# Performance work log

Hardware: AMD Instinct MI355X
Metric: run time of the kernel (lower is better)

The kernel has to match this reference:

```python
import jax, jax.numpy as jnp
import numpy as np

B, H, S, D = 2, 16, 2048, 64
SOFTCLAMP = 50.0


def setup_inputs() -> dict:
    key = jax.random.key(0)
    kq, kk, kv, km = jax.random.split(key, 4)
    q = jax.random.normal(kq, (B, H, S, D), dtype=jnp.float32)
    k = jax.random.normal(kk, (B, H, S, D), dtype=jnp.float32)
    v = jax.random.normal(kv, (B, H, S, D), dtype=jnp.float32)
    mask = jax.random.randint(km, (B, S), 0, 2).astype(jnp.bool_)
    return {"q": q, "k": k, "v": v, "mask": mask}


def reference(q, k, v, mask):
    scale = q.shape[-1] ** -0.5
    # [b, h, i, j] similarity logits
    sim = jnp.einsum('bhid,bhjd->bhij', q, k) * scale
    # tanh-based logit softclamping (Gemma2-style softcapping)
    sim = jnp.tanh(sim / SOFTCLAMP) * SOFTCLAMP
    mask_value = -jnp.finfo(sim.dtype).max
    sim = jnp.where(mask[:, None, None, :], sim, mask_value)
    attn = jax.nn.softmax(sim, axis=-1)
    out = jnp.einsum('bhij,bhjd->bhid', attn, v)
    return out, attn
```

## Files before the change

### kernel.cpp

```cpp
#include <hip/hip_runtime.h>
#include <hip/hip_bf16.h>

#define B_ 2
#define H_ 16
#define S_ 2048
#define D_ 64
#define PSTR 2056

typedef float f32x4 __attribute__((ext_vector_type(4)));
typedef short s16x8 __attribute__((ext_vector_type(8)));
typedef short s16x4 __attribute__((ext_vector_type(4)));

__device__ __forceinline__ short f2bf(float f) {
  unsigned u = __float_as_uint(f);
  u += 0x7FFFu + ((u >> 16) & 1u);
  return (short)(u >> 16);
}
__device__ __forceinline__ float bf2f(short s) {
  return __uint_as_float(((unsigned)(unsigned short)s) << 16);
}

__device__ __forceinline__ float softcap_p(float a) {
  const float k1 = 0.18033688011f;
  const float k2 = -3.7570183e-07f;
  const float k3 = 9.3926761e-13f;
  const float C  = 72.134752044f;
  float y = a * a;
  float t = __builtin_fmaf(y, k3, k2);
  t = __builtin_fmaf(y, t, k1);
  float arg = __builtin_fmaf(a, t, -C);
  arg = fminf(arg, 0.f);
  return exp2f(arg);
}

__global__ __launch_bounds__(256) void prep_qk(const float* __restrict__ q,
                                               const float* __restrict__ k,
                                               short* __restrict__ qbf,
                                               short* __restrict__ kbf) {
  size_t i = ((size_t)blockIdx.x * 256 + threadIdx.x) * 8;
  const f32x4* qa = (const f32x4*)(q + i);
  const f32x4* ka = (const f32x4*)(k + i);
  f32x4 a0 = __builtin_nontemporal_load(qa);
  f32x4 a1 = __builtin_nontemporal_load(qa + 1);
  f32x4 b0 = __builtin_nontemporal_load(ka);
  f32x4 b1 = __builtin_nontemporal_load(ka + 1);
  s16x8 oq, ok;
  #pragma unroll
  for (int e = 0; e < 4; ++e) {
    oq[e] = f2bf(a0[e]); oq[4 + e] = f2bf(a1[e]);
    ok[e] = f2bf(b0[e]); ok[4 + e] = f2bf(b1[e]);
  }
  *(s16x8*)(qbf + i) = oq;
  *(s16x8*)(kbf + i) = ok;
}

__global__ __launch_bounds__(256) void prep_v(const float* __restrict__ v,
                                              short* __restrict__ vt) {
  __shared__ float tile[64][65];
  const int tid = threadIdx.x;
  const int j0 = blockIdx.x * 64;
  const int bh = blockIdx.y;
  const float* vh = v + (size_t)bh * S_ * D_;
  #pragma unroll
  for (int it = 0; it < 16; ++it) {
    int idx = it * 256 + tid;
    int row = idx >> 6, col = idx & 63;
    tile[row][col] = __builtin_nontemporal_load(&vh[(size_t)(j0 + row) * D_ + col]);
  }
  __syncthreads();
  short* vth = vt + (size_t)bh * D_ * S_;
  #pragma unroll
  for (int it = 0; it < 16; ++it) {
    int idx = it * 256 + tid;
    int d = idx >> 6, jj = idx & 63;
    vth[(size_t)d * S_ + j0 + jj] = f2bf(tile[jj][d]);
  }
}

template <bool PRE>
__global__ __launch_bounds__(512, 2) void attend_fused(
    const float* __restrict__ q, const float* __restrict__ k,
    const float* __restrict__ v, const int* __restrict__ mask,
    const short* __restrict__ qbf, const short* __restrict__ kbf,
    const short* __restrict__ vt,
    float* __restrict__ out, float* __restrict__ attn) {
  __shared__ short strip[16 * PSTR];
  __shared__ float ls_rs[8][16];
  __shared__ float ls_rinv[16];

  const int tid  = threadIdx.x;
  const int wv   = tid >> 6;
  const int lane = tid & 63;
  const int lg   = lane >> 4;
  const int li   = lane & 15;

  const unsigned flat = blockIdx.y * gridDim.x + blockIdx.x;
  const unsigned swz  = (flat & 7) * 512 + (flat >> 3);
  const int q0 = (int)(swz & 127) * 16;
  const int bh = (int)(swz >> 7);
  const int b  = bh >> 4;
  const int* mrow = mask + (size_t)b * S_;

  s16x8 qf0, qf1;
  if constexpr (PRE) {
    const short* qr = qbf + ((size_t)bh * S_ + q0 + li) * D_ + lg * 8;
    qf0 = *(const s16x8*)qr;
    qf1 = *(const s16x8*)(qr + 32);
  } else {
    const float* qr = q + ((size_t)bh * S_ + q0 + li) * D_ + lg * 8;
    #pragma unroll
    for (int e = 0; e < 8; ++e) { qf0[e] = f2bf(qr[e]); qf1[e] = f2bf(qr[32 + e]); }
  }

  const short* kbase = PRE ? (kbf + (size_t)bh * S_ * D_) : nullptr;
  s16x8 kf[8];
  auto ldK = [&](int cc) {
    const int jcc = cc * 512 + wv * 64;
    #pragma unroll
    for (int n = 0; n < 4; ++n) {
      const short* kr = kbase + (size_t)(jcc + n * 16 + li) * D_ + lg * 8;
      kf[2 * n]     = *(const s16x8*)kr;
      kf[2 * n + 1] = *(const s16x8*)(kr + 32);
    }
  };
  if constexpr (PRE) ldK(0);

  float rs[4] = {0.f, 0.f, 0.f, 0.f};
  f32x4 pvacc[4];
  #pragma unroll
  for (int m = 0; m < 4; ++m) pvacc[m] = (f32x4){0.f, 0.f, 0.f, 0.f};

  #pragma unroll
  for (int c = 0; c < 4; ++c) {
    const int jc = c * 512 + wv * 64;

    f32x4 acc[4];
    #pragma unroll
    for (int n = 0; n < 4; ++n) acc[n] = (f32x4){0.f, 0.f, 0.f, 0.f};
    if constexpr (PRE) {
      #pragma unroll
      for (int n = 0; n < 4; ++n) {
        acc[n] = __builtin_amdgcn_mfma_f32_16x16x32_bf16(qf0, kf[2 * n], acc[n], 0, 0, 0);
        acc[n] = __builtin_amdgcn_mfma_f32_16x16x32_bf16(qf1, kf[2 * n + 1], acc[n], 0, 0, 0);
      }
      if (c < 3) ldK(c + 1);
    } else {
      #pragma unroll
      for (int n = 0; n < 4; ++n) {
        const float* kr = k + ((size_t)bh * S_ + jc + n * 16 + li) * D_ + lg * 8;
        s16x8 k0, k1;
        #pragma unroll
        for (int e = 0; e < 8; ++e) { k0[e] = f2bf(kr[e]); k1[e] = f2bf(kr[32 + e]); }
        acc[n] = __builtin_amdgcn_mfma_f32_16x16x32_bf16(qf0, k0, acc[n], 0, 0, 0);
        acc[n] = __builtin_amdgcn_mfma_f32_16x16x32_bf16(qf1, k1, acc[n], 0, 0, 0);
      }
    }

    #pragma unroll
    for (int n = 0; n < 4; ++n) {
      const int j = jc + n * 16 + li;
      const bool keep = mrow[j] != 0;
      #pragma unroll
      for (int r = 0; r < 4; ++r) {
        float pp = softcap_p(acc[n][r]);
        float pv_ = keep ? pp : 0.f;
        rs[r] += pv_;
        strip[(lg * 4 + r) * PSTR + j] = f2bf(pv_);
      }
    }

    #pragma unroll
    for (int ks = 0; ks < 2; ++ks) {
      s16x8 pa = *(const s16x8*)&strip[li * PSTR + jc + ks * 32 + lg * 8];
      #pragma unroll
      for (int m = 0; m < 4; ++m) {
        s16x8 vb;
        if constexpr (PRE) {
          vb = *(const s16x8*)(vt + ((size_t)bh * D_ + m * 16 + li) * S_ + jc + ks * 32 + lg * 8);
        } else {
          const float* vp = v + (size_t)bh * S_ * D_ + (size_t)(jc + ks * 32 + lg * 8) * D_ + m * 16 + li;
          #pragma unroll
          for (int e = 0; e < 8; ++e) vb[e] = f2bf(vp[(size_t)e * D_]);
        }
        pvacc[m] = __builtin_amdgcn_mfma_f32_16x16x32_bf16(pa, vb, pvacc[m], 0, 0, 0);
      }
    }
  }

  #pragma unroll
  for (int r = 0; r < 4; ++r) {
    #pragma unroll
    for (int m = 1; m < 16; m <<= 1) rs[r] += __shfl_xor(rs[r], m, 64);
  }
  if (li == 0) {
    #pragma unroll
    for (int r = 0; r < 4; ++r) ls_rs[wv][lg * 4 + r] = rs[r];
  }
  __syncthreads();
  if (tid < 16) {
    float ssum = 0.f;
    #pragma unroll
    for (int w = 0; w < 8; ++w) ssum += ls_rs[w][tid];
    ls_rinv[tid] = (ssum > 0.f) ? 1.f / ssum : 0.f;
  }
  __syncthreads();

  const int row0 = wv * 2, row1 = wv * 2 + 1;
  const float rv0 = ls_rinv[row0], rv1 = ls_rinv[row1];
  s16x4 pb0[8], pb1[8];
  #pragma unroll
  for (int it = 0; it < 8; ++it) {
    pb0[it] = *(const s16x4*)&strip[row0 * PSTR + it * 256 + lane * 4];
    pb1[it] = *(const s16x4*)&strip[row1 * PSTR + it * 256 + lane * 4];
  }
  __syncthreads();

  float (*pvred)[16][64] = (float (*)[16][64])strip;
  #pragma unroll
  for (int m = 0; m < 4; ++m)
    #pragma unroll
    for (int r = 0; r < 4; ++r)
      pvred[wv][lg * 4 + r][m * 16 + li] = pvacc[m][r];
  __syncthreads();

  #pragma unroll
  for (int h = 0; h < 2; ++h) {
    const int idx = h * 512 + tid;
    const int qq = idx >> 6, d = idx & 63;
    float ssum = 0.f;
    #pragma unroll
    for (int w = 0; w < 8; ++w) ssum += pvred[w][qq][d];
    out[((size_t)bh * S_ + q0 + qq) * D_ + d] = ssum * ls_rinv[qq];
  }

  {
    float* abase = attn + ((size_t)bh * S_ + q0) * S_;
    float* arow0 = abase + (size_t)row0 * S_;
    float* arow1 = abase + (size_t)row1 * S_;
    #pragma unroll
    for (int it = 0; it < 8; ++it) {
      f32x4 a0, a1;
      #pragma unroll
      for (int e = 0; e < 4; ++e) {
        a0[e] = bf2f(pb0[it][e]) * rv0;
        a1[e] = bf2f(pb1[it][e]) * rv1;
      }
      *(f32x4*)(arow0 + it * 256 + lane * 4) = a0;
      *(f32x4*)(arow1 + it * 256 + lane * 4) = a1;
    }
  }
}

extern "C" void kernel_launch(void* const* d_in, const int* in_sizes, int n_in,
                              void* d_out, int out_size, void* d_ws, size_t ws_size,
                              hipStream_t stream) {
  const float* q = (const float*)d_in[0];
  const float* k = (const float*)d_in[1];
  const float* v = (const float*)d_in[2];
  const int* mask = (const int*)d_in[3];

  float* out  = (float*)d_out;
  const size_t nel = (size_t)B_ * H_ * S_ * D_;
  float* attn = out + nel;

  dim3 grid(S_ / 16, B_ * H_);
  const size_t need = nel * 2 * 3;

  if (ws_size >= need) {
    short* qbf = (short*)d_ws;
    short* kbf = qbf + nel;
    short* vtp = kbf + nel;
    prep_qk<<<(int)(nel / (256 * 8)), 256, 0, stream>>>(q, k, qbf, kbf);
    prep_v<<<dim3(S_ / 64, B_ * H_), 256, 0, stream>>>(v, vtp);
    attend_fused<true><<<grid, 512, 0, stream>>>(q, k, v, mask, qbf, kbf, vtp, out, attn);
  } else {
    attend_fused<false><<<grid, 512, 0, stream>>>(q, k, v, mask, nullptr, nullptr, nullptr, out, attn);
  }
}
```

Before: 319.8 us.

## Make attention kernel persistent and overlap attn stores with next tile compute

Replaces the one-block-per-query-tile grid with 512 persistent blocks that each process 8 consecutive query tiles. The normalized attention-row stores for the previous tile are deferred and interleaved into the next tile's QK^T loop, so the large fp32 attn write overlaps MFMA work. It also drops the K register prefetch (loading K directly before each MFMA) and raises the launch-bounds occupancy hint from 2 to 4. In exchange it adds an extra barrier per tile, serializes tiles within a block, and register pressure from holding the bf16 strip values across iterations may cause spills under the tighter occupancy hint.

```diff
diff --git a/kernel.cpp b/kernel.cpp
--- a/kernel.cpp
+++ b/kernel.cpp
@@ -78,7 +78,7 @@
 }
 
 template <bool PRE>
-__global__ __launch_bounds__(512, 2) void attend_fused(
+__global__ __launch_bounds__(512, 4) void attend_persist(
     const float* __restrict__ q, const float* __restrict__ k,
     const float* __restrict__ v, const int* __restrict__ mask,
     const short* __restrict__ qbf, const short* __restrict__ kbf,
@@ -94,160 +94,172 @@
   const int lg   = lane >> 4;
   const int li   = lane & 15;
 
-  const unsigned flat = blockIdx.y * gridDim.x + blockIdx.x;
-  const unsigned swz  = (flat & 7) * 512 + (flat >> 3);
-  const int q0 = (int)(swz & 127) * 16;
-  const int bh = (int)(swz >> 7);
-  const int b  = bh >> 4;
-  const int* mrow = mask + (size_t)b * S_;
-
-  s16x8 qf0, qf1;
-  if constexpr (PRE) {
-    const short* qr = qbf + ((size_t)bh * S_ + q0 + li) * D_ + lg * 8;
-    qf0 = *(const s16x8*)qr;
-    qf1 = *(const s16x8*)(qr + 32);
-  } else {
-    const float* qr = q + ((size_t)bh * S_ + q0 + li) * D_ + lg * 8;
-    #pragma unroll
-    for (int e = 0; e < 8; ++e) { qf0[e] = f2bf(qr[e]); qf1[e] = f2bf(qr[32 + e]); }
-  }
-
-  const short* kbase = PRE ? (kbf + (size_t)bh * S_ * D_) : nullptr;
-  s16x8 kf[8];
-  auto ldK = [&](int cc) {
-    const int jcc = cc * 512 + wv * 64;
-    #pragma unroll
-    for (int n = 0; n < 4; ++n) {
-      const short* kr = kbase + (size_t)(jcc + n * 16 + li) * D_ + lg * 8;
-      kf[2 * n]     = *(const s16x8*)kr;
-      kf[2 * n + 1] = *(const s16x8*)(kr + 32);
-    }
-  };
-  if constexpr (PRE) ldK(0);
-
-  float rs[4] = {0.f, 0.f, 0.f, 0.f};
-  f32x4 pvacc[4];
-  #pragma unroll
-  for (int m = 0; m < 4; ++m) pvacc[m] = (f32x4){0.f, 0.f, 0.f, 0.f};
-
-  #pragma unroll
-  for (int c = 0; c < 4; ++c) {
-    const int jc = c * 512 + wv * 64;
-
-    f32x4 acc[4];
-    #pragma unroll
-    for (int n = 0; n < 4; ++n) acc[n] = (f32x4){0.f, 0.f, 0.f, 0.f};
+  const int linear = (int)(blockIdx.x & 7) * 64 + (int)(blockIdx.x >> 3);
+
+  s16x4 pb0[8], pb1[8];
+  float rv0 = 0.f, rv1 = 0.f;
+  float* arow0p = nullptr;
+  float* arow1p = nullptr;
+
+  #pragma unroll 1
+  for (int t = 0; t < 8; ++t) {
+    const int tile_id = linear * 8 + t;
+    const int bh = tile_id >> 7;
+    const int q0 = (tile_id & 127) * 16;
+    const int b  = bh >> 4;
+    const int* mrow = mask + (size_t)b * S_;
+
+    s16x8 qf0, qf1;
     if constexpr (PRE) {
+      const short* qr = qbf + ((size_t)bh * S_ + q0 + li) * D_ + lg * 8;
+      qf0 = *(const s16x8*)qr;
+      qf1 = *(const s16x8*)(qr + 32);
+    } else {
+      const float* qr = q + ((size_t)bh * S_ + q0 + li) * D_ + lg * 8;
+      #pragma unroll
+      for (int e = 0; e < 8; ++e) { qf0[e] = f2bf(qr[e]); qf1[e] = f2bf(qr[32 + e]); }
+    }
+
+    const short* kbase = PRE ? (kbf + (size_t)bh * S_ * D_) : nullptr;
+    const short* vbase = PRE ? (vt + (size_t)bh * D_ * S_) : nullptr;
+
+    float rs[4] = {0.f, 0.f, 0.f, 0.f};
+    f32x4 pvacc[4];
+    #pragma unroll
+    for (int m = 0; m < 4; ++m) pvacc[m] = (f32x4){0.f, 0.f, 0.f, 0.f};
+
+    #pragma unroll
+    for (int c = 0; c < 4; ++c) {
+      const int jc = c * 512 + wv * 64;
+
+      f32x4 acc[4];
+      #pragma unroll
+      for (int n = 0; n < 4; ++n) acc[n] = (f32x4){0.f, 0.f, 0.f, 0.f};
       #pragma unroll
       for (int n = 0; n < 4; ++n) {
-        acc[n] = __builtin_amdgcn_mfma_f32_16x16x32_bf16(qf0, kf[2 * n], acc[n], 0, 0, 0);
-        acc[n] = __builtin_amdgcn_mfma_f32_16x16x32_bf16(qf1, kf[2 * n + 1], acc[n], 0, 0, 0);
-      }
-      if (c < 3) ldK(c + 1);
-    } else {
+        if constexpr (PRE) {
+          const short* kr = kbase + (size_t)(jc + n * 16 + li) * D_ + lg * 8;
+          acc[n] = __builtin_amdgcn_mfma_f32_16x16x32_bf16(qf0, *(const s16x8*)kr, acc[n], 0, 0, 0);
+          acc[n] = __builtin_amdgcn_mfma_f32_16x16x32_bf16(qf1, *(const s16x8*)(kr + 32), acc[n], 0, 0, 0);
+        } else {
+          const float* kr = k + ((size_t)bh * S_ + jc + n * 16 + li) * D_ + lg * 8;
+          s16x8 k0, k1;
+          #pragma unroll
+          for (int e = 0; e < 8; ++e) { k0[e] = f2bf(kr[e]); k1[e] = f2bf(kr[32 + e]); }
+          acc[n] = __builtin_amdgcn_mfma_f32_16x16x32_bf16(qf0, k0, acc[n], 0, 0, 0);
+          acc[n] = __builtin_amdgcn_mfma_f32_16x16x32_bf16(qf1, k1, acc[n], 0, 0, 0);
+        }
+      }
+
+      if (t > 0) {
+        #pragma unroll
+        for (int h = 0; h < 2; ++h) {
+          const int it = c + h * 4;
+          f32x4 a0, a1;
+          #pragma unroll
+          for (int e = 0; e < 4; ++e) {
+            a0[e] = bf2f(pb0[it][e]) * rv0;
+            a1[e] = bf2f(pb1[it][e]) * rv1;
+          }
+          *(f32x4*)(arow0p + it * 256 + lane * 4) = a0;
+          *(f32x4*)(arow1p + it * 256 + lane * 4) = a1;
+        }
+      }
+
       #pragma unroll
       for (int n = 0; n < 4; ++n) {
-        const float* kr = k + ((size_t)bh * S_ + jc + n * 16 + li) * D_ + lg * 8;
-        s16x8 k0, k1;
+        const int j = jc + n * 16 + li;
+        const bool keep = mrow[j] != 0;
         #pragma unroll
-        for (int e = 0; e < 8; ++e) { k0[e] = f2bf(kr[e]); k1[e] = f2bf(kr[32 + e]); }
-        acc[n] = __builtin_amdgcn_mfma_f32_16x16x32_bf16(qf0, k0, acc[n], 0, 0, 0);
-        acc[n] = __builtin_amdgcn_mfma_f32_16x16x32_bf16(qf1, k1, acc[n], 0, 0, 0);
-      }
-    }
-
-    #pragma unroll
-    for (int n = 0; n < 4; ++n) {
-      const int j = jc + n * 16 + li;
-      const bool keep = mrow[j] != 0;
-      #pragma unroll
-      for (int r = 0; r < 4; ++r) {
-        float pp = softcap_p(acc[n][r]);
-        float pv_ = keep ? pp : 0.f;
-        rs[r] += pv_;
-        strip[(lg * 4 + r) * PSTR + j] = f2bf(pv_);
-      }
-    }
-
-    #pragma unroll
-    for (int ks = 0; ks < 2; ++ks) {
-      s16x8 pa = *(const s16x8*)&strip[li * PSTR + jc + ks * 32 + lg * 8];
-      #pragma unroll
-      for (int m = 0; m < 4; ++m) {
-        s16x8 vb;
-        if constexpr (PRE) {
-          vb = *(const s16x8*)(vt + ((size_t)bh * D_ + m * 16 + li) * S_ + jc + ks * 32 + lg * 8);
-        } else {
-          const float* vp = v + (size_t)bh * S_ * D_ + (size_t)(jc + ks * 32 + lg * 8) * D_ + m * 16 + li;
-          #pragma unroll
-          for (int e = 0; e < 8; ++e) vb[e] = f2bf(vp[(size_t)e * D_]);
-        }
-        pvacc[m] = __builtin_amdgcn_mfma_f32_16x16x32_bf16(pa, vb, pvacc[m], 0, 0, 0);
-      }
-    }
-  }
-
-  #pragma unroll
-  for (int r = 0; r < 4; ++r) {
-    #pragma unroll
-    for (int m = 1; m < 16; m <<= 1) rs[r] += __shfl_xor(rs[r], m, 64);
-  }
-  if (li == 0) {
-    #pragma unroll
-    for (int r = 0; r < 4; ++r) ls_rs[wv][lg * 4 + r] = rs[r];
-  }
-  __syncthreads();
-  if (tid < 16) {
-    float ssum = 0.f;
-    #pragma unroll
-    for (int w = 0; w < 8; ++w) ssum += ls_rs[w][tid];
-    ls_rinv[tid] = (ssum > 0.f) ? 1.f / ssum : 0.f;
-  }
-  __syncthreads();
-
-  const int row0 = wv * 2, row1 = wv * 2 + 1;
-  const float rv0 = ls_rinv[row0], rv1 = ls_rinv[row1];
-  s16x4 pb0[8], pb1[8];
+        for (int r = 0; r < 4; ++r) {
+          float pp = softcap_p(acc[n][r]);
+          float pv_ = keep ? pp : 0.f;
+          rs[r] += pv_;
+          strip[(lg * 4 + r) * PSTR + j] = f2bf(pv_);
+        }
+      }
+
+      #pragma unroll
+      for (int ks = 0; ks < 2; ++ks) {
+        s16x8 pa = *(const s16x8*)&strip[li * PSTR + jc + ks * 32 + lg * 8];
+        #pragma unroll
+        for (int m = 0; m < 4; ++m) {
+          s16x8 vb;
+          if constexpr (PRE) {
+            vb = *(const s16x8*)(vbase + (size_t)(m * 16 + li) * S_ + jc + ks * 32 + lg * 8);
+          } else {
+            const float* vp = v + (size_t)bh * S_ * D_ + (size_t)(jc + ks * 32 + lg * 8) * D_ + m * 16 + li;
+            #pragma unroll
+            for (int e = 0; e < 8; ++e) vb[e] = f2bf(vp[(size_t)e * D_]);
+          }
+          pvacc[m] = __builtin_amdgcn_mfma_f32_16x16x32_bf16(pa, vb, pvacc[m], 0, 0, 0);
+        }
+      }
+    }
+
+    #pragma unroll
+    for (int r = 0; r < 4; ++r) {
+      #pragma unroll
+      for (int m = 1; m < 16; m <<= 1) rs[r] += __shfl_xor(rs[r], m, 64);
+    }
+    if (li == 0) {
+      #pragma unroll
+      for (int r = 0; r < 4; ++r) ls_rs[wv][lg * 4 + r] = rs[r];
+    }
+    __syncthreads();
+    if (tid < 16) {
+      float ssum = 0.f;
+      #pragma unroll
+      for (int w = 0; w < 8; ++w) ssum += ls_rs[w][tid];
+      ls_rinv[tid] = (ssum > 0.f) ? 1.f / ssum : 0.f;
+    }
+    __syncthreads();
+
+    const int row0 = wv * 2, row1 = wv * 2 + 1;
+    rv0 = ls_rinv[row0];
+    rv1 = ls_rinv[row1];
+    #pragma unroll
+    for (int it = 0; it < 8; ++it) {
+      pb0[it] = *(const s16x4*)&strip[row0 * PSTR + it * 256 + lane * 4];
+      pb1[it] = *(const s16x4*)&strip[row1 * PSTR + it * 256 + lane * 4];
+    }
+    {
+      float* abase = attn + ((size_t)bh * S_ + q0) * S_;
+      arow0p = abase + (size_t)row0 * S_;
+      arow1p = abase + (size_t)row1 * S_;
+    }
+    __syncthreads();
+
+    float (*pvred)[16][64] = (float (*)[16][64])strip;
+    #pragma unroll
+    for (int m = 0; m < 4; ++m)
+      #pragma unroll
+      for (int r = 0; r < 4; ++r)
+        pvred[wv][lg * 4 + r][m * 16 + li] = pvacc[m][r];
+    __syncthreads();
+
+    #pragma unroll
+    for (int h = 0; h < 2; ++h) {
+      const int idx = h * 512 + tid;
+      const int qq = idx >> 6, d = idx & 63;
+      float ssum = 0.f;
+      #pragma unroll
+      for (int w = 0; w < 8; ++w) ssum += pvred[w][qq][d];
+      out[((size_t)bh * S_ + q0 + qq) * D_ + d] = ssum * ls_rinv[qq];
+    }
+    __syncthreads();
+  }
+
   #pragma unroll
   for (int it = 0; it < 8; ++it) {
-    pb0[it] = *(const s16x4*)&strip[row0 * PSTR + it * 256 + lane * 4];
-    pb1[it] = *(const s16x4*)&strip[row1 * PSTR + it * 256 + lane * 4];
-  }
-  __syncthreads();
-
-  float (*pvred)[16][64] = (float (*)[16][64])strip;
-  #pragma unroll
-  for (int m = 0; m < 4; ++m)
-    #pragma unroll
-    for (int r = 0; r < 4; ++r)
-      pvred[wv][lg * 4 + r][m * 16 + li] = pvacc[m][r];
-  __syncthreads();
-
-  #pragma unroll
-  for (int h = 0; h < 2; ++h) {
-    const int idx = h * 512 + tid;
-    const int qq = idx >> 6, d = idx & 63;
-    float ssum = 0.f;
-    #pragma unroll
-    for (int w = 0; w < 8; ++w) ssum += pvred[w][qq][d];
-    out[((size_t)bh * S_ + q0 + qq) * D_ + d] = ssum * ls_rinv[qq];
-  }
-
-  {
-    float* abase = attn + ((size_t)bh * S_ + q0) * S_;
-    float* arow0 = abase + (size_t)row0 * S_;
-    float* arow1 = abase + (size_t)row1 * S_;
-    #pragma unroll
-    for (int it = 0; it < 8; ++it) {
-      f32x4 a0, a1;
-      #pragma unroll
-      for (int e = 0; e < 4; ++e) {
-        a0[e] = bf2f(pb0[it][e]) * rv0;
-        a1[e] = bf2f(pb1[it][e]) * rv1;
-      }
-      *(f32x4*)(arow0 + it * 256 + lane * 4) = a0;
-      *(f32x4*)(arow1 + it * 256 + lane * 4) = a1;
-    }
+    f32x4 a0, a1;
+    #pragma unroll
+    for (int e = 0; e < 4; ++e) {
+      a0[e] = bf2f(pb0[it][e]) * rv0;
+      a1[e] = bf2f(pb1[it][e]) * rv1;
+    }
+    *(f32x4*)(arow0p + it * 256 + lane * 4) = a0;
+    *(f32x4*)(arow1p + it * 256 + lane * 4) = a1;
   }
 }
 
@@ -263,7 +275,6 @@
   const size_t nel = (size_t)B_ * H_ * S_ * D_;
   float* attn = out + nel;
 
-  dim3 grid(S_ / 16, B_ * H_);
   const size_t need = nel * 2 * 3;
 
   if (ws_size >= need) {
@@ -272,8 +283,8 @@
     short* vtp = kbf + nel;
     prep_qk<<<(int)(nel / (256 * 8)), 256, 0, stream>>>(q, k, qbf, kbf);
     prep_v<<<dim3(S_ / 64, B_ * H_), 256, 0, stream>>>(v, vtp);
-    attend_fused<true><<<grid, 512, 0, stream>>>(q, k, v, mask, qbf, kbf, vtp, out, attn);
+    attend_persist<true><<<512, 512, 0, stream>>>(q, k, v, mask, qbf, kbf, vtp, out, attn);
   } else {
-    attend_fused<false><<<grid, 512, 0, stream>>>(q, k, v, mask, nullptr, nullptr, nullptr, out, attn);
-  }
-}
+    attend_persist<false><<<512, 512, 0, stream>>>(q, k, v, mask, nullptr, nullptr, nullptr, out, attn);
+  }
+}
```

After: 659.8 us. 2.06x slower.
